# Kernel tuning notes

Measured on AMD Instinct MI355X. Metric: run time of the kernel, lower is better.

## Reference

```python
import jax, jax.numpy as jnp
import numpy as np

H, DH, CHUNK = 8, 64, 64      # heads, dim_head, chunk_size
DIM = 512
INNER = H * DH                # 512
EPS = 1e-5
SCALE = DH ** -0.5


def _ln(x, g, b):
    m = jnp.mean(x, -1, keepdims=True)
    v = jnp.mean((x - m) ** 2, -1, keepdims=True)
    return (x - m) * jax.lax.rsqrt(v + EPS) * g + b


def _heads(t):
    b, n, _ = t.shape
    return t.reshape(b, n, H, DH).transpose(0, 2, 1, 3)  # b h n d


def _merge(t):
    b, h, n, d = t.shape
    return t.transpose(0, 2, 1, 3).reshape(b, n, h * d)  # b n (h d)


def _local_attn(x, W_qkv, W_ao, b_ao):
    # PreNorm inner Attention: non-overlapping chunked local self-attention
    qkv = x @ W_qkv
    q, k, v = (jnp.split(qkv, 3, axis=-1))
    q, k, v = _heads(q), _heads(k), _heads(v)
    B, Hh, N, D = q.shape
    M = N // CHUNK
    qc = q.reshape(B, Hh, M, CHUNK, D)
    kc = k.reshape(B, Hh, M, CHUNK, D)
    vc = v.reshape(B, Hh, M, CHUNK, D)
    s = jnp.einsum('bhmcd,bhmkd->bhmck', qc, kc) * SCALE
    a = jax.nn.softmax(s, axis=-1)
    o = jnp.einsum('bhmck,bhmkd->bhmcd', a, vc).reshape(B, Hh, N, D)
    return _merge(o) @ W_ao + b_ao


def setup_inputs() -> dict:
    key = jax.random.key(0)
    ks = jax.random.split(key, 10)
    p = lambda k, shp: jax.random.normal(k, shp, dtype=jnp.float32) * 0.02
    return {
        'x':     jax.random.normal(ks[0], (2, 4096, DIM), dtype=jnp.float32),
        'q_x':   jax.random.normal(ks[1], (2, 2048, DIM), dtype=jnp.float32),
        'ln1_g': jnp.ones((DIM,), jnp.float32),
        'ln1_b': jnp.zeros((DIM,), jnp.float32),
        'W_qkv': p(ks[2], (DIM, INNER * 3)),
        'W_ao':  p(ks[3], (INNER, DIM)),
        'b_ao':  jnp.zeros((DIM,), jnp.float32),
        'ln2_g': jnp.ones((DIM,), jnp.float32),
        'ln2_b': jnp.zeros((DIM,), jnp.float32),
        'W_q':   p(ks[4], (DIM, INNER)),
        'W_kv':  p(ks[5], (DIM, INNER * 2)),
        'W_o':   p(ks[6], (INNER, DIM)),
        'b_o':   jnp.zeros((DIM,), jnp.float32),
    }


def reference(x, q_x, ln1_g, ln1_b, W_qkv, W_ao, b_ao,
              ln2_g, ln2_b, W_q, W_kv, W_o, b_o):
    # inner chunked self-attn with PreNorm + residual
    q_in = _local_attn(_ln(q_x, ln1_g, ln1_b), W_qkv, W_ao, b_ao) + q_x
    q_in = _ln(q_in, ln2_g, ln2_b)
    # full cross-attention: queries from q_in, keys/values from x
    q = _heads(q_in @ W_q)
    k, v = jnp.split(x @ W_kv, 2, axis=-1)
    k, v = _heads(k), _heads(v)
    s = jnp.einsum('bhqd,bhkd->bhqk', q, k) * SCALE
    a = jax.nn.softmax(s, axis=-1)
    out = _merge(jnp.einsum('bhqk,bhkd->bhqd', a, v)) @ W_o + b_o
    return (out, q_in)
```

## Files before the change

### kernel.cpp

```cpp
#include <hip/hip_runtime.h>

typedef unsigned short u16;
typedef unsigned int u32;
typedef __attribute__((ext_vector_type(4))) float f32x4;
typedef __attribute__((ext_vector_type(8))) __bf16 bf16x8;

#define NQ 2048
#define NK 4096
#define SCALE 0.125f
#define LOG2E 1.44269504088896f

__device__ __forceinline__ u16 f2bf(float f) {
  u32 x = __float_as_uint(f);
  return (u16)((x + 0x7fffu + ((x >> 16) & 1u)) >> 16);
}

__device__ __forceinline__ float bf2f(u16 b) {
  return __uint_as_float(((u32)b) << 16);
}

__device__ __forceinline__ int swz(int row, int colbyte) {
  return row * 128 + (colbyte ^ ((row & 7) << 4));
}

__device__ __forceinline__ void async16(u16* lds, const u16* g) {
  __builtin_amdgcn_global_load_lds(
      (const __attribute__((address_space(1))) void*)g,
      (__attribute__((address_space(3))) void*)lds, 16, 0, 0);
}

__device__ __forceinline__ f32x4 mfma16(bf16x8 a, bf16x8 b, f32x4 c) {
  return __builtin_amdgcn_mfma_f32_16x16x32_bf16(a, b, c, 0, 0, 0);
}

__device__ __forceinline__ float max16(const f32x4* s) {
  float a = fmaxf(fmaxf(s[0][0], s[0][1]), fmaxf(s[0][2], s[0][3]));
  float b = fmaxf(fmaxf(s[1][0], s[1][1]), fmaxf(s[1][2], s[1][3]));
  float c = fmaxf(fmaxf(s[2][0], s[2][1]), fmaxf(s[2][2], s[2][3]));
  float d = fmaxf(fmaxf(s[3][0], s[3][1]), fmaxf(s[3][2], s[3][3]));
  return fmaxf(fmaxf(a, b), fmaxf(c, d));
}

__global__ __launch_bounds__(256) void k_prep(
    const float* __restrict__ Wqkv, const float* __restrict__ Wao,
    const float* __restrict__ Wq, const float* __restrict__ Wkv,
    const float* __restrict__ Wo, const float* __restrict__ x,
    const float* __restrict__ qx, const float* __restrict__ ln1g,
    const float* __restrict__ ln1b,
    u16* __restrict__ o_qkv, u16* __restrict__ o_ao, u16* __restrict__ o_q,
    u16* __restrict__ o_kv, u16* __restrict__ o_o, u16* __restrict__ x_bf,
    u16* __restrict__ xn_bf) {
  int bid = blockIdx.x;
  int t = threadIdx.x;
  if (bid < 8192) {
    int idx = bid * 256 + t;
    int r = idx >> 9, k = idx & 511;
    const float* in;
    u16* out;
    int N, n;
    if (r < 1536)      { in = Wqkv; out = o_qkv; N = 1536; n = r; }
    else if (r < 2048) { in = Wao;  out = o_ao;  N = 512;  n = r - 1536; }
    else if (r < 2560) { in = Wq;   out = o_q;   N = 512;  n = r - 2048; }
    else if (r < 3584) { in = Wkv;  out = o_kv;  N = 1024; n = r - 2560; }
    else               { in = Wo;   out = o_o;   N = 512;  n = r - 3584; }
    out[(size_t)n * 512 + k] = f2bf(in[(size_t)k * N + n]);
  } else if (bid < 10240) {
    size_t i = ((size_t)(bid - 8192) * 256 + t) * 8;
    float v[8];
    *(float4*)&v[0] = *(const float4*)(x + i);
    *(float4*)&v[4] = *(const float4*)(x + i + 4);
    u16 o[8];
#pragma unroll
    for (int j = 0; j < 8; j++) o[j] = f2bf(v[j]);
    *(uint4*)(x_bf + i) = *(uint4*)o;
  } else {
    int row = (bid - 10240) * 4 + (t >> 6);
    int lane = t & 63;
    size_t base = (size_t)row * 512 + lane * 8;
    float v[8];
    *(float4*)&v[0] = *(const float4*)(qx + base);
    *(float4*)&v[4] = *(const float4*)(qx + base + 4);
    float s = 0.f, q = 0.f;
#pragma unroll
    for (int j = 0; j < 8; j++) { s += v[j]; q += v[j] * v[j]; }
#pragma unroll
    for (int d = 1; d < 64; d <<= 1) {
      s += __shfl_xor(s, d, 64);
      q += __shfl_xor(q, d, 64);
    }
    float mean = s * (1.f / 512.f);
    float var = q * (1.f / 512.f) - mean * mean;
    float rstd = rsqrtf(var + 1e-5f);
    float gv[8], bv[8];
    *(float4*)&gv[0] = *(const float4*)(ln1g + lane * 8);
    *(float4*)&gv[4] = *(const float4*)(ln1g + lane * 8 + 4);
    *(float4*)&bv[0] = *(const float4*)(ln1b + lane * 8);
    *(float4*)&bv[4] = *(const float4*)(ln1b + lane * 8 + 4);
    u16 ob[8];
#pragma unroll
    for (int j = 0; j < 8; j++)
      ob[j] = f2bf((v[j] - mean) * rstd * gv[j] + bv[j]);
    *(uint4*)(xn_bf + base) = *(uint4*)ob;
  }
}

__global__ __launch_bounds__(64) void k_ln(const float* __restrict__ xin,
                                           const float* __restrict__ res,
                                           const float* __restrict__ gg,
                                           const float* __restrict__ bb,
                                           float* __restrict__ fout,
                                           u16* __restrict__ bfout) {
  int row = blockIdx.x, t = threadIdx.x;
  size_t base = (size_t)row * 512 + t * 8;
  float v[8];
  *(float4*)&v[0] = *(const float4*)(xin + base);
  *(float4*)&v[4] = *(const float4*)(xin + base + 4);
  if (res) {
    float r2[8];
    *(float4*)&r2[0] = *(const float4*)(res + base);
    *(float4*)&r2[4] = *(const float4*)(res + base + 4);
#pragma unroll
    for (int j = 0; j < 8; j++) v[j] += r2[j];
  }
  float s = 0.f, q = 0.f;
#pragma unroll
  for (int j = 0; j < 8; j++) { s += v[j]; q += v[j] * v[j]; }
#pragma unroll
  for (int d = 1; d < 64; d <<= 1) {
    s += __shfl_xor(s, d, 64);
    q += __shfl_xor(q, d, 64);
  }
  float mean = s * (1.f / 512.f);
  float var = q * (1.f / 512.f) - mean * mean;
  float rstd = rsqrtf(var + 1e-5f);
  float gv[8], bv[8];
  *(float4*)&gv[0] = *(const float4*)(gg + t * 8);
  *(float4*)&gv[4] = *(const float4*)(gg + t * 8 + 4);
  *(float4*)&bv[0] = *(const float4*)(bb + t * 8);
  *(float4*)&bv[4] = *(const float4*)(bb + t * 8 + 4);
  float y[8];
  u16 ob[8];
#pragma unroll
  for (int j = 0; j < 8; j++) {
    y[j] = (v[j] - mean) * rstd * gv[j] + bv[j];
    ob[j] = f2bf(y[j]);
  }
  if (fout) {
    *(float4*)(fout + base) = *(float4*)&y[0];
    *(float4*)(fout + base + 4) = *(float4*)&y[4];
  }
  if (bfout) *(uint4*)(bfout + base) = *(uint4*)ob;
}

template <bool BIAS, bool OBF16, bool KVPACK>
__global__ __launch_bounds__(256) void k_gemm(const u16* __restrict__ A,
                                              const u16* __restrict__ Bt,
                                              const float* __restrict__ bias,
                                              void* __restrict__ C,
                                              void* __restrict__ C2,
                                              int M, int N, int K) {
  __shared__ u16 As[8192];
  __shared__ u16 Bs[8192];
  const int tid = threadIdx.x;
  const int lane = tid & 63, wid = tid >> 6;
  const int lr = lane & 15, g = lane >> 4;
  const int wr = wid >> 1, wc = wid & 1;
  const int rowBase = blockIdx.y * 128, colBase = blockIdx.x * 128;
  f32x4 acc[4][4] = {};
  const int srow = wid * 8 + (lane >> 3);
  const int scol = ((lane & 7) ^ (lane >> 3)) << 3;
  const u16* gA = A + (size_t)(rowBase + srow) * K + scol;
  const u16* gB = Bt + (size_t)(colBase + srow) * K + scol;
  u16* lA = As + wid * 512;
  u16* lB = Bs + wid * 512;
  const size_t rK = (size_t)32 * K;
  for (int k0 = 0; k0 < K; k0 += 64) {
#pragma unroll
    for (int r = 0; r < 4; r++) async16(lA + r * 2048, gA + r * rK + k0);
#pragma unroll
    for (int r = 0; r < 4; r++) async16(lB + r * 2048, gB + r * rK + k0);
    __syncthreads();
#pragma unroll
    for (int kk = 0; kk < 2; kk++) {
      bf16x8 af[4], bw[4];
#pragma unroll
      for (int fm = 0; fm < 4; fm++) {
        int row = wr * 64 + fm * 16 + lr;
        af[fm] = *(const bf16x8*)((const char*)As + row * 128 +
                                  (((kk * 4 + g) ^ (row & 7)) << 4));
      }
#pragma unroll
      for (int fn = 0; fn < 4; fn++) {
        int row = wc * 64 + fn * 16 + lr;
        bw[fn] = *(const bf16x8*)((const char*)Bs + row * 128 +
                                  (((kk * 4 + g) ^ (row & 7)) << 4));
      }
#pragma unroll
      for (int fm = 0; fm < 4; fm++)
#pragma unroll
        for (int fn = 0; fn < 4; fn++)
          acc[fm][fn] = mfma16(af[fm], bw[fn], acc[fm][fn]);
    }
    __syncthreads();
  }
#pragma unroll
  for (int fm = 0; fm < 4; fm++) {
#pragma unroll
    for (int fn = 0; fn < 4; fn++) {
      int row = rowBase + wr * 64 + fm * 16 + g * 4;
      int col = colBase + wc * 64 + fn * 16 + lr;
      if constexpr (KVPACK) {
        int b = row >> 12, n = row & 4095, kt = n >> 6, key0 = n & 63;
        int h = (col >> 6) & 7, d = col & 63;
        size_t tbase = ((size_t)(((b << 3) + h) << 6) + kt) * 4096;
        if (col < 512) {
          u16* kd = (u16*)C + tbase + (size_t)key0 * 64 + d;
          kd[0] = f2bf(acc[fm][fn][0]);
          kd[64] = f2bf(acc[fm][fn][1]);
          kd[128] = f2bf(acc[fm][fn][2]);
          kd[192] = f2bf(acc[fm][fn][3]);
        } else {
          u16 p4[4] = {f2bf(acc[fm][fn][0]), f2bf(acc[fm][fn][1]),
                       f2bf(acc[fm][fn][2]), f2bf(acc[fm][fn][3])};
          *(uint2*)((u16*)C2 + tbase + (size_t)d * 64 + key0) = *(uint2*)p4;
        }
      } else {
        float bvv = BIAS ? bias[col] : 0.f;
#pragma unroll
        for (int r = 0; r < 4; r++) {
          float v = acc[fm][fn][r] + bvv;
          if (OBF16)
            ((u16*)C)[(size_t)(row + r) * N + col] = f2bf(v);
          else
            ((float*)C)[(size_t)(row + r) * N + col] = v;
        }
      }
    }
  }
}

template <bool BIAS, bool OBF16>
__global__ __launch_bounds__(256) void k_gemm2(const u16* __restrict__ A,
                                               const u16* __restrict__ Bt,
                                               const float* __restrict__ bias,
                                               void* __restrict__ C, int M, int N, int K) {
  __shared__ u16 As[4096];
  __shared__ u16 Bs[8192];
  const int tid = threadIdx.x;
  const int lane = tid & 63, wid = tid >> 6;
  const int lr = lane & 15, g = lane >> 4;
  const int wr = wid >> 1, wc = wid & 1;
  const int rowBase = blockIdx.y * 64, colBase = blockIdx.x * 128;
  f32x4 acc[2][4] = {};
  const int srow = wid * 8 + (lane >> 3);
  const int scol = ((lane & 7) ^ (lane >> 3)) << 3;
  const u16* gA = A + (size_t)(rowBase + srow) * K + scol;
  const u16* gB = Bt + (size_t)(colBase + srow) * K + scol;
  u16* lA = As + wid * 512;
  u16* lB = Bs + wid * 512;
  const size_t rK = (size_t)32 * K;
  for (int k0 = 0; k0 < K; k0 += 64) {
#pragma unroll
    for (int r = 0; r < 2; r++) async16(lA + r * 2048, gA + r * rK + k0);
#pragma unroll
    for (int r = 0; r < 4; r++) async16(lB + r * 2048, gB + r * rK + k0);
    __syncthreads();
#pragma unroll
    for (int kk = 0; kk < 2; kk++) {
      bf16x8 af[2], bw[4];
#pragma unroll
      for (int fm = 0; fm < 2; fm++) {
        int row = wr * 32 + fm * 16 + lr;
        af[fm] = *(const bf16x8*)((const char*)As + row * 128 +
                                  (((kk * 4 + g) ^ (row & 7)) << 4));
      }
#pragma unroll
      for (int fn = 0; fn < 4; fn++) {
        int row = wc * 64 + fn * 16 + lr;
        bw[fn] = *(const bf16x8*)((const char*)Bs + row * 128 +
                                  (((kk * 4 + g) ^ (row & 7)) << 4));
      }
#pragma unroll
      for (int fm = 0; fm < 2; fm++)
#pragma unroll
        for (int fn = 0; fn < 4; fn++)
          acc[fm][fn] = mfma16(af[fm], bw[fn], acc[fm][fn]);
    }
    __syncthreads();
  }
#pragma unroll
  for (int fm = 0; fm < 2; fm++) {
#pragma unroll
    for (int fn = 0; fn < 4; fn++) {
      int row = rowBase + wr * 32 + fm * 16 + g * 4;
      int col = colBase + wc * 64 + fn * 16 + lr;
      float bvv = BIAS ? bias[col] : 0.f;
#pragma unroll
      for (int r = 0; r < 4; r++) {
        float v = acc[fm][fn][r] + bvv;
        if (OBF16)
          ((u16*)C)[(size_t)(row + r) * N + col] = f2bf(v);
        else
          ((float*)C)[(size_t)(row + r) * N + col] = v;
      }
    }
  }
}

__global__ __launch_bounds__(256) void k_local(const u16* __restrict__ qkv,
                                               u16* __restrict__ oattn) {
  int bid = blockIdx.x;
  int m = bid & 31, h = (bid >> 5) & 7, b = bid >> 8;
  __shared__ u16 Qs[4096], Ks[4096], Vt[4096], Ps[4096];
  int t = threadIdx.x;
  {
    int i = t >> 2, c0 = (t & 3) * 16;
    const u16* base = qkv + (size_t)(b * NQ + m * 64 + i) * 1536 + c0;
    uint4 q0 = *(const uint4*)(base + h * 64);
    uint4 q1 = *(const uint4*)(base + h * 64 + 8);
    uint4 k0 = *(const uint4*)(base + 512 + h * 64);
    uint4 k1 = *(const uint4*)(base + 512 + h * 64 + 8);
    uint4 v0 = *(const uint4*)(base + 1024 + h * 64);
    uint4 v1 = *(const uint4*)(base + 1024 + h * 64 + 8);
    *(uint4*)((char*)Qs + swz(i, c0 * 2)) = q0;
    *(uint4*)((char*)Qs + swz(i, c0 * 2 + 16)) = q1;
    *(uint4*)((char*)Ks + swz(i, c0 * 2)) = k0;
    *(uint4*)((char*)Ks + swz(i, c0 * 2 + 16)) = k1;
    u16 vv[16];
    *(uint4*)&vv[0] = v0;
    *(uint4*)&vv[8] = v1;
#pragma unroll
    for (int j = 0; j < 16; j++) {
      int d = c0 + j;
      *(u16*)((char*)Vt + swz(d, i * 2)) = vv[j];
    }
  }
  __syncthreads();
  int lane = t & 63, w = t >> 6, lr = lane & 15, g = lane >> 4;
  bf16x8 aq[2];
#pragma unroll
  for (int kk = 0; kk < 2; kk++)
    aq[kk] = *(const bf16x8*)((const char*)Qs + swz(w * 16 + lr, kk * 64 + g * 16));
  f32x4 s[4] = {};
#pragma unroll
  for (int fn = 0; fn < 4; fn++)
#pragma unroll
    for (int kk = 0; kk < 2; kk++) {
      bf16x8 bk = *(const bf16x8*)((const char*)Ks + swz(fn * 16 + lr, kk * 64 + g * 16));
      s[fn] = mfma16(aq[kk], bk, s[fn]);
    }
  float mx[4], sm[4], p[4][4];
#pragma unroll
  for (int r = 0; r < 4; r++)
    mx[r] = fmaxf(fmaxf(s[0][r], s[1][r]), fmaxf(s[2][r], s[3][r]));
#pragma unroll
  for (int d = 1; d < 16; d <<= 1)
#pragma unroll
    for (int r = 0; r < 4; r++) mx[r] = fmaxf(mx[r], __shfl_xor(mx[r], d, 64));
#pragma unroll
  for (int r = 0; r < 4; r++) {
    float a = 0.f;
#pragma unroll
    for (int fn = 0; fn < 4; fn++) {
      p[fn][r] = exp2f((s[fn][r] - mx[r]) * (SCALE * LOG2E));
      a += p[fn][r];
    }
    sm[r] = a;
  }
#pragma unroll
  for (int d = 1; d < 16; d <<= 1)
#pragma unroll
    for (int r = 0; r < 4; r++) sm[r] += __shfl_xor(sm[r], d, 64);
  float rinv[4];
#pragma unroll
  for (int r = 0; r < 4; r++) rinv[r] = 1.f / sm[r];
#pragma unroll
  for (int fn = 0; fn < 4; fn++)
#pragma unroll
    for (int r = 0; r < 4; r++)
      *(u16*)((char*)Ps + swz(w * 16 + g * 4 + r, (fn * 16 + lr) * 2)) =
          f2bf(p[fn][r] * rinv[r]);
  bf16x8 ap[2];
#pragma unroll
  for (int kk = 0; kk < 2; kk++)
    ap[kk] = *(const bf16x8*)((const char*)Ps + swz(w * 16 + lr, kk * 64 + g * 16));
  f32x4 o[4] = {};
#pragma unroll
  for (int fn = 0; fn < 4; fn++)
#pragma unroll
    for (int kk = 0; kk < 2; kk++) {
      bf16x8 bv = *(const bf16x8*)((const char*)Vt + swz(fn * 16 + lr, kk * 64 + g * 16));
      o[fn] = mfma16(ap[kk], bv, o[fn]);
    }
#pragma unroll
  for (int fn = 0; fn < 4; fn++)
#pragma unroll
    for (int r = 0; r < 4; r++)
      oattn[(size_t)(b * NQ + m * 64 + w * 16 + g * 4 + r) * 512 + h * 64 + fn * 16 + lr] =
          f2bf(o[fn][r]);
}

__global__ __launch_bounds__(256, 4) void k_cross(const u16* __restrict__ q,
                                                  const u16* __restrict__ kpk,
                                                  const u16* __restrict__ vtp,
                                                  u16* __restrict__ opart,
                                                  float* __restrict__ ml) {
  int f = blockIdx.x + 16 * blockIdx.y + 256 * blockIdx.z;
  int xcd = f & 7, j = f >> 3;
  int c = xcd + 8 * (j >> 4);
  int qt = j & 15, bh = c & 15, split = c >> 4;
  int b = bh >> 3, h = bh & 7;
  int t = threadIdx.x, lane = t & 63, w = t >> 6, lr = lane & 15, g = lane >> 4;
  __shared__ u16 Ks[3][4096], Vs[2][4096], Ps[4096];
  u16* pw = Ps + w * 1024;
  const float cs = SCALE * LOG2E;

  bf16x8 ones;
#pragma unroll
  for (int i = 0; i < 8; i++) ones[i] = (__bf16)1.0f;

  int srow = w * 16 + (lane >> 3);
  int soff0 = srow * 64 + (((lane & 7) ^ (srow & 7)) << 3);
  int soff1 = soff0 + 512;
  const u16* ktiles = kpk + ((size_t)(bh * 64 + split * 16) * 4096);
  const u16* vtiles = vtp + ((size_t)(bh * 64 + split * 16) * 4096);

  const u16* qrowL = q + (size_t)(b * NQ + qt * 128 + w * 32 + lr) * 512 + h * 64;
  const u16* qrowH = qrowL + 16 * 512;
  bf16x8 aqL0 = *(const bf16x8*)(qrowL + g * 8);
  bf16x8 aqL1 = *(const bf16x8*)(qrowL + 32 + g * 8);
  bf16x8 aqH0 = *(const bf16x8*)(qrowH + g * 8);
  bf16x8 aqH1 = *(const bf16x8*)(qrowH + 32 + g * 8);

  f32x4 oL[4] = {}, oH[4] = {};
  f32x4 lsumL = {}, lsumH = {};
  float mL = -1e30f, mH = -1e30f;

  async16(&Vs[0][w * 1024], vtiles + soff0);
  async16(&Vs[0][w * 1024 + 512], vtiles + soff1);
  async16(&Ks[0][w * 1024], ktiles + soff0);
  async16(&Ks[0][w * 1024 + 512], ktiles + soff1);
  async16(&Ks[1][w * 1024], ktiles + 4096 + soff0);
  async16(&Ks[1][w * 1024 + 512], ktiles + 4096 + soff1);

  int kb = 0, ksb = 2, vb = 0;
  for (int kt = 0; kt < 16; kt++) {
    if (kt < 15) {
      asm volatile("s_waitcnt vmcnt(2)" ::: "memory");
    } else {
      asm volatile("s_waitcnt vmcnt(0)" ::: "memory");
    }
    __builtin_amdgcn_sched_barrier(0);
    __builtin_amdgcn_s_barrier();
    __builtin_amdgcn_sched_barrier(0);
    if (kt < 15) {
      const u16* vn = vtiles + (size_t)(kt + 1) * 4096;
      async16(&Vs[vb ^ 1][w * 1024], vn + soff0);
      async16(&Vs[vb ^ 1][w * 1024 + 512], vn + soff1);
    }
    if (kt < 14) {
      const u16* kn = ktiles + (size_t)(kt + 2) * 4096;
      async16(&Ks[ksb][w * 1024], kn + soff0);
      async16(&Ks[ksb][w * 1024 + 512], kn + soff1);
    }
    f32x4 stL[4], stH[4];
    __builtin_amdgcn_s_setprio(1);
#pragma unroll
    for (int fm = 0; fm < 4; fm++) {
      bf16x8 bk0 = *(const bf16x8*)((const char*)Ks[kb] + swz(fm * 16 + lr, g * 16));
      bf16x8 bk1 = *(const bf16x8*)((const char*)Ks[kb] + swz(fm * 16 + lr, 64 + g * 16));
      stL[fm] = mfma16(bk0, aqL0, (f32x4){0.f, 0.f, 0.f, 0.f});
      stL[fm] = mfma16(bk1, aqL1, stL[fm]);
      stH[fm] = mfma16(bk0, aqH0, (f32x4){0.f, 0.f, 0.f, 0.f});
      stH[fm] = mfma16(bk1, aqH1, stH[fm]);
    }
    __builtin_amdgcn_s_setprio(0);
    float tmL = max16(stL);
    tmL = fmaxf(tmL, __shfl_xor(tmL, 16, 64));
    tmL = fmaxf(tmL, __shfl_xor(tmL, 32, 64));
    if (!__all(tmL <= mL + 22.2f)) {
      float mnew = fmaxf(mL, tmL);
      float corr = exp2f((mL - mnew) * cs);
      mL = mnew;
      float c0 = __shfl(corr, g * 4 + 0, 64);
      float c1 = __shfl(corr, g * 4 + 1, 64);
      float c2 = __shfl(corr, g * 4 + 2, 64);
      float c3 = __shfl(corr, g * 4 + 3, 64);
      lsumL[0] *= c0; lsumL[1] *= c1; lsumL[2] *= c2; lsumL[3] *= c3;
#pragma unroll
      for (int fn = 0; fn < 4; fn++) {
        oL[fn][0] *= c0; oL[fn][1] *= c1; oL[fn][2] *= c2; oL[fn][3] *= c3;
      }
    }
    {
      float mc = mL * cs;
#pragma unroll
      for (int fm = 0; fm < 4; fm++) {
        float p0 = exp2f(stL[fm][0] * cs - mc);
        float p1 = exp2f(stL[fm][1] * cs - mc);
        float p2 = exp2f(stL[fm][2] * cs - mc);
        float p3 = exp2f(stL[fm][3] * cs - mc);
        union { __bf16 hh[4]; uint2 vv; } pu;
        pu.hh[0] = (__bf16)p0; pu.hh[1] = (__bf16)p1;
        pu.hh[2] = (__bf16)p2; pu.hh[3] = (__bf16)p3;
        *(uint2*)((char*)pw + swz(lr, fm * 32 + g * 8)) = pu.vv;
      }
    }
    bf16x8 apL0 = *(const bf16x8*)((const char*)pw + swz(lr, g * 16));
    bf16x8 apL1 = *(const bf16x8*)((const char*)pw + swz(lr, 64 + g * 16));
    float tmH = max16(stH);
    tmH = fmaxf(tmH, __shfl_xor(tmH, 16, 64));
    tmH = fmaxf(tmH, __shfl_xor(tmH, 32, 64));
    if (!__all(tmH <= mH + 22.2f)) {
      float mnew = fmaxf(mH, tmH);
      float corr = exp2f((mH - mnew) * cs);
      mH = mnew;
      float c0 = __shfl(corr, g * 4 + 0, 64);
      float c1 = __shfl(corr, g * 4 + 1, 64);
      float c2 = __shfl(corr, g * 4 + 2, 64);
      float c3 = __shfl(corr, g * 4 + 3, 64);
      lsumH[0] *= c0; lsumH[1] *= c1; lsumH[2] *= c2; lsumH[3] *= c3;
#pragma unroll
      for (int fn = 0; fn < 4; fn++) {
        oH[fn][0] *= c0; oH[fn][1] *= c1; oH[fn][2] *= c2; oH[fn][3] *= c3;
      }
    }
    {
      float mc = mH * cs;
#pragma unroll
      for (int fm = 0; fm < 4; fm++) {
        float p0 = exp2f(stH[fm][0] * cs - mc);
        float p1 = exp2f(stH[fm][1] * cs - mc);
        float p2 = exp2f(stH[fm][2] * cs - mc);
        float p3 = exp2f(stH[fm][3] * cs - mc);
        union { __bf16 hh[4]; uint2 vv; } pu;
        pu.hh[0] = (__bf16)p0; pu.hh[1] = (__bf16)p1;
        pu.hh[2] = (__bf16)p2; pu.hh[3] = (__bf16)p3;
        *(uint2*)((char*)pw + swz(lr, fm * 32 + g * 8)) = pu.vv;
      }
    }
    bf16x8 apH0 = *(const bf16x8*)((const char*)pw + swz(lr, g * 16));
    bf16x8 apH1 = *(const bf16x8*)((const char*)pw + swz(lr, 64 + g * 16));
    __builtin_amdgcn_s_setprio(1);
    lsumL = mfma16(apL0, ones, lsumL);
    lsumL = mfma16(apL1, ones, lsumL);
    lsumH = mfma16(apH0, ones, lsumH);
    lsumH = mfma16(apH1, ones, lsumH);
#pragma unroll
    for (int fn = 0; fn < 4; fn++) {
      bf16x8 bv0 = *(const bf16x8*)((const char*)Vs[vb] + swz(fn * 16 + lr, g * 16));
      bf16x8 bv1 = *(const bf16x8*)((const char*)Vs[vb] + swz(fn * 16 + lr, 64 + g * 16));
      oL[fn] = mfma16(apL0, bv0, oL[fn]);
      oL[fn] = mfma16(apL1, bv1, oL[fn]);
      oH[fn] = mfma16(apH0, bv0, oH[fn]);
      oH[fn] = mfma16(apH1, bv1, oH[fn]);
    }
    __builtin_amdgcn_s_setprio(0);
    kb = (kb == 2) ? 0 : kb + 1;
    ksb = (ksb == 2) ? 0 : ksb + 1;
    vb ^= 1;
  }
  size_t sb = ((size_t)(split * 16 + bh) * NQ) + qt * 128 + w * 32;
  {
    float r0 = 1.f / lsumL[0], r1 = 1.f / lsumL[1];
    float r2 = 1.f / lsumL[2], r3 = 1.f / lsumL[3];
#pragma unroll
    for (int fn = 0; fn < 4; fn++) {
      opart[(sb + g * 4 + 0) * 64 + fn * 16 + lr] = f2bf(oL[fn][0] * r0);
      opart[(sb + g * 4 + 1) * 64 + fn * 16 + lr] = f2bf(oL[fn][1] * r1);
      opart[(sb + g * 4 + 2) * 64 + fn * 16 + lr] = f2bf(oL[fn][2] * r2);
      opart[(sb + g * 4 + 3) * 64 + fn * 16 + lr] = f2bf(oL[fn][3] * r3);
    }
  }
  {
    float r0 = 1.f / lsumH[0], r1 = 1.f / lsumH[1];
    float r2 = 1.f / lsumH[2], r3 = 1.f / lsumH[3];
#pragma unroll
    for (int fn = 0; fn < 4; fn++) {
      opart[(sb + 16 + g * 4 + 0) * 64 + fn * 16 + lr] = f2bf(oH[fn][0] * r0);
      opart[(sb + 16 + g * 4 + 1) * 64 + fn * 16 + lr] = f2bf(oH[fn][1] * r1);
      opart[(sb + 16 + g * 4 + 2) * 64 + fn * 16 + lr] = f2bf(oH[fn][2] * r2);
      opart[(sb + 16 + g * 4 + 3) * 64 + fn * 16 + lr] = f2bf(oH[fn][3] * r3);
    }
  }
  if (g == 0) {
    ml[(sb + lr) * 2] = mL;
    ml[(sb + 16 + lr) * 2] = mH;
  }
  if (lr == 0) {
#pragma unroll
    for (int r = 0; r < 4; r++) {
      ml[(sb + g * 4 + r) * 2 + 1] = lsumL[r];
      ml[(sb + 16 + g * 4 + r) * 2 + 1] = lsumH[r];
    }
  }
}

__global__ __launch_bounds__(256) void k_comb(const u16* __restrict__ opart,
                                              const float* __restrict__ ml,
                                              u16* __restrict__ co) {
  int idx = blockIdx.x * 256 + threadIdx.x;
  int c8 = idx & 7;
  int row = (idx >> 3) & 2047;
  int bh = idx >> 14;
  int b = bh >> 3, h = bh & 7;
  const float cs = SCALE * LOG2E;
  float m[4], l[4];
#pragma unroll
  for (int s = 0; s < 4; s++) {
    size_t rb = ((size_t)(s * 16 + bh) * NQ + row);
    m[s] = ml[rb * 2];
    l[s] = ml[rb * 2 + 1];
  }
  float M = fmaxf(fmaxf(m[0], m[1]), fmaxf(m[2], m[3]));
  float wsum = 0.f, wgt[4];
#pragma unroll
  for (int s = 0; s < 4; s++) {
    wgt[s] = l[s] * exp2f((m[s] - M) * cs);
    wsum += wgt[s];
  }
  float acc[8] = {};
#pragma unroll
  for (int s = 0; s < 4; s++) {
    size_t rb = ((size_t)(s * 16 + bh) * NQ + row);
    uint4 pk = *(const uint4*)(opart + rb * 64 + c8 * 8);
    u16 pe[8];
    *(uint4*)pe = pk;
#pragma unroll
    for (int j = 0; j < 8; j++) acc[j] += wgt[s] * bf2f(pe[j]);
  }
  float rw = 1.f / wsum;
  u16 ob[8];
#pragma unroll
  for (int j = 0; j < 8; j++) ob[j] = f2bf(acc[j] * rw);
  *(uint4*)(co + ((size_t)(b * NQ + row) * 512) + h * 64 + c8 * 8) = *(uint4*)ob;
}

extern "C" void kernel_launch(void* const* d_in, const int* in_sizes, int n_in,
                              void* d_out, int out_size, void* d_ws, size_t ws_size,
                              hipStream_t stream) {
  const float* x    = (const float*)d_in[0];
  const float* qx   = (const float*)d_in[1];
  const float* ln1g = (const float*)d_in[2];
  const float* ln1b = (const float*)d_in[3];
  const float* Wqkv = (const float*)d_in[4];
  const float* Wao  = (const float*)d_in[5];
  const float* bao  = (const float*)d_in[6];
  const float* ln2g = (const float*)d_in[7];
  const float* ln2b = (const float*)d_in[8];
  const float* Wq   = (const float*)d_in[9];
  const float* Wkv  = (const float*)d_in[10];
  const float* Wo   = (const float*)d_in[11];
  const float* bo   = (const float*)d_in[12];
  float* out_p = (float*)d_out;
  float* qin_p = out_p + (size_t)2 * 2048 * 512;

  const size_t MiB = 1048576;
  char* ws = (char*)d_ws;
  u16* w_qkv_t = (u16*)(ws);
  u16* w_ao_t  = (u16*)(ws + 1572864);
  u16* w_q_t   = (u16*)(ws + 2097152);
  u16* w_kv_t  = (u16*)(ws + 2621440);
  u16* w_o_t   = (u16*)(ws + 3670016);
  u16* kpk     = (u16*)(ws + 4 * MiB);
  u16* vtp     = (u16*)(ws + 12 * MiB);
  u16* x_bf    = (u16*)(ws + 20 * MiB);
  u16* oattn_bf = (u16*)(ws + 20 * MiB);
  float* ao_f  = (float*)(ws + 24 * MiB);
  u16* xn_bf   = (u16*)(ws + 28 * MiB);
  u16* qin_bf  = (u16*)(ws + 32 * MiB);
  u16* opart   = (u16*)(ws + 20 * MiB);
  u16* qkv_bf  = (u16*)(ws + 36 * MiB);
  u16* q_bf    = (u16*)(ws + 36 * MiB);
  u16* co_bf   = (u16*)(ws + 40 * MiB);
  float* ml    = out_p;

  k_prep<<<dim3(8192 + 2048 + 1024), 256, 0, stream>>>(
      Wqkv, Wao, Wq, Wkv, Wo, x, qx, ln1g, ln1b,
      w_qkv_t, w_ao_t, w_q_t, w_kv_t, w_o_t, x_bf, xn_bf);
  k_gemm<false, true, true><<<dim3(1024 / 128, 8192 / 128), 256, 0, stream>>>(
      x_bf, w_kv_t, nullptr, kpk, vtp, 8192, 1024, 512);
  k_gemm2<false, true><<<dim3(1536 / 128, 4096 / 64), 256, 0, stream>>>(
      xn_bf, w_qkv_t, nullptr, qkv_bf, 4096, 1536, 512);
  k_local<<<dim3(512), 256, 0, stream>>>(qkv_bf, oattn_bf);
  k_gemm2<true, false><<<dim3(512 / 128, 4096 / 64), 256, 0, stream>>>(
      oattn_bf, w_ao_t, bao, ao_f, 4096, 512, 512);
  k_ln<<<dim3(4096), 64, 0, stream>>>(ao_f, qx, ln2g, ln2b, qin_p, qin_bf);
  k_gemm2<false, true><<<dim3(512 / 128, 4096 / 64), 256, 0, stream>>>(
      qin_bf, w_q_t, nullptr, q_bf, 4096, 512, 512);
  k_cross<<<dim3(16, 16, 4), 256, 0, stream>>>(q_bf, kpk, vtp, opart, ml);
  k_comb<<<dim3(262144 / 256), 256, 0, stream>>>(opart, ml, co_bf);
  k_gemm2<true, false><<<dim3(512 / 128, 4096 / 64), 256, 0, stream>>>(
      co_bf, w_o_t, bo, out_p, 4096, 512, 512);
}
```

Measured before the change: 173.5 us.

## Merge KV and QKV projection GEMMs into one launch; simplify cross-attn pipeline

Combines the KV-projection GEMM and the QKV-projection GEMM into a single kernel launch that dispatches on block index, so the two independent GEMMs share the GPU and one launch plus its tail is removed. Separately, the cross-attention kernel drops its triple-buffered K with manual vmcnt waits and raw barriers, and uses plain double buffering of K and V with __syncthreads. This cuts LDS use and code complexity, but the K prefetch distance shrinks and a full barrier now sits at the end of every iteration, which may expose load latency.

```diff
diff --git a/kernel.cpp b/kernel.cpp
--- a/kernel.cpp
+++ b/kernel.cpp
@@ -152,69 +152,68 @@
   if (bfout) *(uint4*)(bfout + base) = *(uint4*)ob;
 }
 
-template <bool BIAS, bool OBF16, bool KVPACK>
-__global__ __launch_bounds__(256) void k_gemm(const u16* __restrict__ A,
-                                              const u16* __restrict__ Bt,
-                                              const float* __restrict__ bias,
-                                              void* __restrict__ C,
-                                              void* __restrict__ C2,
-                                              int M, int N, int K) {
+__global__ __launch_bounds__(256) void k_mm0(
+    const u16* __restrict__ xb, const u16* __restrict__ wkv,
+    const u16* __restrict__ xn, const u16* __restrict__ wqkv,
+    u16* __restrict__ kpk, u16* __restrict__ vtp, u16* __restrict__ qkv) {
   __shared__ u16 As[8192];
   __shared__ u16 Bs[8192];
   const int tid = threadIdx.x;
   const int lane = tid & 63, wid = tid >> 6;
   const int lr = lane & 15, g = lane >> 4;
   const int wr = wid >> 1, wc = wid & 1;
-  const int rowBase = blockIdx.y * 128, colBase = blockIdx.x * 128;
-  f32x4 acc[4][4] = {};
   const int srow = wid * 8 + (lane >> 3);
   const int scol = ((lane & 7) ^ (lane >> 3)) << 3;
-  const u16* gA = A + (size_t)(rowBase + srow) * K + scol;
-  const u16* gB = Bt + (size_t)(colBase + srow) * K + scol;
   u16* lA = As + wid * 512;
   u16* lB = Bs + wid * 512;
-  const size_t rK = (size_t)32 * K;
-  for (int k0 = 0; k0 < K; k0 += 64) {
-#pragma unroll
-    for (int r = 0; r < 4; r++) async16(lA + r * 2048, gA + r * rK + k0);
-#pragma unroll
-    for (int r = 0; r < 4; r++) async16(lB + r * 2048, gB + r * rK + k0);
-    __syncthreads();
-#pragma unroll
-    for (int kk = 0; kk < 2; kk++) {
-      bf16x8 af[4], bw[4];
-#pragma unroll
-      for (int fm = 0; fm < 4; fm++) {
-        int row = wr * 64 + fm * 16 + lr;
-        af[fm] = *(const bf16x8*)((const char*)As + row * 128 +
-                                  (((kk * 4 + g) ^ (row & 7)) << 4));
-      }
+  const size_t rK = (size_t)32 * 512;
+  int bid = blockIdx.x;
+  if (bid < 512) {
+    int bx = bid & 7, by = bid >> 3;
+    const int rowBase = by * 128, colBase = bx * 128;
+    f32x4 acc[4][4] = {};
+    const u16* gA = xb + (size_t)(rowBase + srow) * 512 + scol;
+    const u16* gB = wkv + (size_t)(colBase + srow) * 512 + scol;
+    for (int k0 = 0; k0 < 512; k0 += 64) {
+#pragma unroll
+      for (int r = 0; r < 4; r++) async16(lA + r * 2048, gA + r * rK + k0);
+#pragma unroll
+      for (int r = 0; r < 4; r++) async16(lB + r * 2048, gB + r * rK + k0);
+      __syncthreads();
+#pragma unroll
+      for (int kk = 0; kk < 2; kk++) {
+        bf16x8 af[4], bw[4];
+#pragma unroll
+        for (int fm = 0; fm < 4; fm++) {
+          int row = wr * 64 + fm * 16 + lr;
+          af[fm] = *(const bf16x8*)((const char*)As + row * 128 +
+                                    (((kk * 4 + g) ^ (row & 7)) << 4));
+        }
+#pragma unroll
+        for (int fn = 0; fn < 4; fn++) {
+          int row = wc * 64 + fn * 16 + lr;
+          bw[fn] = *(const bf16x8*)((const char*)Bs + row * 128 +
+                                    (((kk * 4 + g) ^ (row & 7)) << 4));
+        }
+#pragma unroll
+        for (int fm = 0; fm < 4; fm++)
+#pragma unroll
+          for (int fn = 0; fn < 4; fn++)
+            acc[fm][fn] = mfma16(af[fm], bw[fn], acc[fm][fn]);
+      }
+      __syncthreads();
+    }
+#pragma unroll
+    for (int fm = 0; fm < 4; fm++) {
 #pragma unroll
       for (int fn = 0; fn < 4; fn++) {
-        int row = wc * 64 + fn * 16 + lr;
-        bw[fn] = *(const bf16x8*)((const char*)Bs + row * 128 +
-                                  (((kk * 4 + g) ^ (row & 7)) << 4));
-      }
-#pragma unroll
-      for (int fm = 0; fm < 4; fm++)
-#pragma unroll
-        for (int fn = 0; fn < 4; fn++)
-          acc[fm][fn] = mfma16(af[fm], bw[fn], acc[fm][fn]);
-    }
-    __syncthreads();
-  }
-#pragma unroll
-  for (int fm = 0; fm < 4; fm++) {
-#pragma unroll
-    for (int fn = 0; fn < 4; fn++) {
-      int row = rowBase + wr * 64 + fm * 16 + g * 4;
-      int col = colBase + wc * 64 + fn * 16 + lr;
-      if constexpr (KVPACK) {
+        int row = rowBase + wr * 64 + fm * 16 + g * 4;
+        int col = colBase + wc * 64 + fn * 16 + lr;
         int b = row >> 12, n = row & 4095, kt = n >> 6, key0 = n & 63;
         int h = (col >> 6) & 7, d = col & 63;
         size_t tbase = ((size_t)(((b << 3) + h) << 6) + kt) * 4096;
         if (col < 512) {
-          u16* kd = (u16*)C + tbase + (size_t)key0 * 64 + d;
+          u16* kd = kpk + tbase + (size_t)key0 * 64 + d;
           kd[0] = f2bf(acc[fm][fn][0]);
           kd[64] = f2bf(acc[fm][fn][1]);
           kd[128] = f2bf(acc[fm][fn][2]);
@@ -222,18 +221,55 @@
         } else {
           u16 p4[4] = {f2bf(acc[fm][fn][0]), f2bf(acc[fm][fn][1]),
                        f2bf(acc[fm][fn][2]), f2bf(acc[fm][fn][3])};
-          *(uint2*)((u16*)C2 + tbase + (size_t)d * 64 + key0) = *(uint2*)p4;
+          *(uint2*)(vtp + tbase + (size_t)d * 64 + key0) = *(uint2*)p4;
         }
-      } else {
-        float bvv = BIAS ? bias[col] : 0.f;
-#pragma unroll
-        for (int r = 0; r < 4; r++) {
-          float v = acc[fm][fn][r] + bvv;
-          if (OBF16)
-            ((u16*)C)[(size_t)(row + r) * N + col] = f2bf(v);
-          else
-            ((float*)C)[(size_t)(row + r) * N + col] = v;
+      }
+    }
+  } else {
+    int j = bid - 512;
+    int bx = j % 12, by = j / 12;
+    const int rowBase = by * 64, colBase = bx * 128;
+    f32x4 acc[2][4] = {};
+    const u16* gA = xn + (size_t)(rowBase + srow) * 512 + scol;
+    const u16* gB = wqkv + (size_t)(colBase + srow) * 512 + scol;
+    for (int k0 = 0; k0 < 512; k0 += 64) {
+#pragma unroll
+      for (int r = 0; r < 2; r++) async16(lA + r * 2048, gA + r * rK + k0);
+#pragma unroll
+      for (int r = 0; r < 4; r++) async16(lB + r * 2048, gB + r * rK + k0);
+      __syncthreads();
+#pragma unroll
+      for (int kk = 0; kk < 2; kk++) {
+        bf16x8 af[2], bw[4];
+#pragma unroll
+        for (int fm = 0; fm < 2; fm++) {
+          int row = wr * 32 + fm * 16 + lr;
+          af[fm] = *(const bf16x8*)((const char*)As + row * 128 +
+                                    (((kk * 4 + g) ^ (row & 7)) << 4));
         }
+#pragma unroll
+        for (int fn = 0; fn < 4; fn++) {
+          int row = wc * 64 + fn * 16 + lr;
+          bw[fn] = *(const bf16x8*)((const char*)Bs + row * 128 +
+                                    (((kk * 4 + g) ^ (row & 7)) << 4));
+        }
+#pragma unroll
+        for (int fm = 0; fm < 2; fm++)
+#pragma unroll
+          for (int fn = 0; fn < 4; fn++)
+            acc[fm][fn] = mfma16(af[fm], bw[fn], acc[fm][fn]);
+      }
+      __syncthreads();
+    }
+#pragma unroll
+    for (int fm = 0; fm < 2; fm++) {
+#pragma unroll
+      for (int fn = 0; fn < 4; fn++) {
+        int row = rowBase + wr * 32 + fm * 16 + g * 4;
+        int col = colBase + wc * 64 + fn * 16 + lr;
+#pragma unroll
+        for (int r = 0; r < 4; r++)
+          qkv[(size_t)(row + r) * 1536 + col] = f2bf(acc[fm][fn][r]);
       }
     }
   }
@@ -411,7 +447,7 @@
   int qt = j & 15, bh = c & 15, split = c >> 4;
   int b = bh >> 3, h = bh & 7;
   int t = threadIdx.x, lane = t & 63, w = t >> 6, lr = lane & 15, g = lane >> 4;
-  __shared__ u16 Ks[3][4096], Vs[2][4096], Ps[4096];
+  __shared__ u16 Ks[2][4096], Vs[2][4096], Ps[4096];
   u16* pw = Ps + w * 1024;
   const float cs = SCALE * LOG2E;
 
@@ -436,39 +472,28 @@
   f32x4 lsumL = {}, lsumH = {};
   float mL = -1e30f, mH = -1e30f;
 
+  async16(&Ks[0][w * 1024], ktiles + soff0);
+  async16(&Ks[0][w * 1024 + 512], ktiles + soff1);
   async16(&Vs[0][w * 1024], vtiles + soff0);
   async16(&Vs[0][w * 1024 + 512], vtiles + soff1);
-  async16(&Ks[0][w * 1024], ktiles + soff0);
-  async16(&Ks[0][w * 1024 + 512], ktiles + soff1);
-  async16(&Ks[1][w * 1024], ktiles + 4096 + soff0);
-  async16(&Ks[1][w * 1024 + 512], ktiles + 4096 + soff1);
-
-  int kb = 0, ksb = 2, vb = 0;
+  __syncthreads();
+
+  int buf = 0;
   for (int kt = 0; kt < 16; kt++) {
     if (kt < 15) {
-      asm volatile("s_waitcnt vmcnt(2)" ::: "memory");
-    } else {
-      asm volatile("s_waitcnt vmcnt(0)" ::: "memory");
-    }
-    __builtin_amdgcn_sched_barrier(0);
-    __builtin_amdgcn_s_barrier();
-    __builtin_amdgcn_sched_barrier(0);
-    if (kt < 15) {
+      const u16* kn = ktiles + (size_t)(kt + 1) * 4096;
       const u16* vn = vtiles + (size_t)(kt + 1) * 4096;
-      async16(&Vs[vb ^ 1][w * 1024], vn + soff0);
-      async16(&Vs[vb ^ 1][w * 1024 + 512], vn + soff1);
-    }
-    if (kt < 14) {
-      const u16* kn = ktiles + (size_t)(kt + 2) * 4096;
-      async16(&Ks[ksb][w * 1024], kn + soff0);
-      async16(&Ks[ksb][w * 1024 + 512], kn + soff1);
+      async16(&Ks[buf ^ 1][w * 1024], kn + soff0);
+      async16(&Ks[buf ^ 1][w * 1024 + 512], kn + soff1);
+      async16(&Vs[buf ^ 1][w * 1024], vn + soff0);
+      async16(&Vs[buf ^ 1][w * 1024 + 512], vn + soff1);
     }
     f32x4 stL[4], stH[4];
     __builtin_amdgcn_s_setprio(1);
 #pragma unroll
     for (int fm = 0; fm < 4; fm++) {
-      bf16x8 bk0 = *(const bf16x8*)((const char*)Ks[kb] + swz(fm * 16 + lr, g * 16));
-      bf16x8 bk1 = *(const bf16x8*)((const char*)Ks[kb] + swz(fm * 16 + lr, 64 + g * 16));
+      bf16x8 bk0 = *(const bf16x8*)((const char*)Ks[buf] + swz(fm * 16 + lr, g * 16));
+      bf16x8 bk1 = *(const bf16x8*)((const char*)Ks[buf] + swz(fm * 16 + lr, 64 + g * 16));
       stL[fm] = mfma16(bk0, aqL0, (f32x4){0.f, 0.f, 0.f, 0.f});
       stL[fm] = mfma16(bk1, aqL1, stL[fm]);
       stH[fm] = mfma16(bk0, aqH0, (f32x4){0.f, 0.f, 0.f, 0.f});
@@ -548,17 +573,16 @@
     lsumH = mfma16(apH1, ones, lsumH);
 #pragma unroll
     for (int fn = 0; fn < 4; fn++) {
-      bf16x8 bv0 = *(const bf16x8*)((const char*)Vs[vb] + swz(fn * 16 + lr, g * 16));
-      bf16x8 bv1 = *(const bf16x8*)((const char*)Vs[vb] + swz(fn * 16 + lr, 64 + g * 16));
+      bf16x8 bv0 = *(const bf16x8*)((const char*)Vs[buf] + swz(fn * 16 + lr, g * 16));
+      bf16x8 bv1 = *(const bf16x8*)((const char*)Vs[buf] + swz(fn * 16 + lr, 64 + g * 16));
       oL[fn] = mfma16(apL0, bv0, oL[fn]);
       oL[fn] = mfma16(apL1, bv1, oL[fn]);
       oH[fn] = mfma16(apH0, bv0, oH[fn]);
       oH[fn] = mfma16(apH1, bv1, oH[fn]);
     }
     __builtin_amdgcn_s_setprio(0);
-    kb = (kb == 2) ? 0 : kb + 1;
-    ksb = (ksb == 2) ? 0 : ksb + 1;
-    vb ^= 1;
+    __syncthreads();
+    buf ^= 1;
   }
   size_t sb = ((size_t)(split * 16 + bh) * NQ) + qt * 128 + w * 32;
   {
@@ -675,13 +699,12 @@
   u16* co_bf   = (u16*)(ws + 40 * MiB);
   float* ml    = out_p;
 
+
   k_prep<<<dim3(8192 + 2048 + 1024), 256, 0, stream>>>(
       Wqkv, Wao, Wq, Wkv, Wo, x, qx, ln1g, ln1b,
       w_qkv_t, w_ao_t, w_q_t, w_kv_t, w_o_t, x_bf, xn_bf);
-  k_gemm<false, true, true><<<dim3(1024 / 128, 8192 / 128), 256, 0, stream>>>(
-      x_bf, w_kv_t, nullptr, kpk, vtp, 8192, 1024, 512);
-  k_gemm2<false, true><<<dim3(1536 / 128, 4096 / 64), 256, 0, stream>>>(
-      xn_bf, w_qkv_t, nullptr, qkv_bf, 4096, 1536, 512);
+  k_mm0<<<dim3(512 + 768), 256, 0, stream>>>(
+      x_bf, w_kv_t, xn_bf, w_qkv_t, kpk, vtp, qkv_bf);
   k_local<<<dim3(512), 256, 0, stream>>>(qkv_bf, oattn_bf);
   k_gemm2<true, false><<<dim3(512 / 128, 4096 / 64), 256, 0, stream>>>(
       oattn_bf, w_ao_t, bao, ao_f, 4096, 512, 512);
```

After: 158.8 us. 1.09x faster.
